# Optimization experiments

Hardware: AMD Instinct MI355X
Metric: run time of the kernel (lower is better)

The kernel has to match this reference:

```python
import jax, jax.numpy as jnp
import numpy as np

EPSILON = 1e-36


def setup_inputs() -> dict:
    key = jax.random.key(0)
    k1, k2, k3, k4 = jax.random.split(key, 4)
    n, in_dim, out_dim = 8192, 128, 128
    x = jax.random.normal(k1, (n, in_dim), dtype=jnp.float32)
    # xavier-uniform-like scale for W_real
    limit = float(np.sqrt(6.0 / (in_dim + out_dim)))
    W_real = jax.random.uniform(k2, (in_dim, out_dim), dtype=jnp.float32, minval=-limit, maxval=limit)
    W_imag = jax.random.uniform(k3, (in_dim, out_dim), dtype=jnp.float32, minval=-0.1, maxval=0.1)
    G = jax.random.uniform(k4, (in_dim, out_dim), dtype=jnp.float32, minval=0.0, maxval=1.0)
    return {"x": x, "W_real": W_real, "W_imag": W_imag, "G": G}


def reference(x, W_real, W_imag, G):
    Gc = jnp.clip(G, 0.0, 1.0)                                   # (i,o)
    # R: (n,i,o) = |x| gated toward 1 by (1-G)
    R = (jnp.abs(x) + EPSILON)[:, :, None] * Gc[None] + (1.0 - Gc)[None]
    # K: pi where x<0, gated by G
    K = jnp.pi * (x < 0).astype(x.dtype)[:, :, None] * Gc[None]  # (n,i,o)
    logR = jnp.log(R)
    A = jnp.einsum('nio,io->no', logR, W_real) - jnp.einsum('nio,io->no', K, W_imag)
    B = jnp.einsum('nio,io->no', logR, W_imag) + jnp.einsum('nio,io->no', K, W_real)
    return jnp.exp(A) * jnp.cos(B)
```

## Files before the change

kernel.cpp:

```cpp
#include <hip/hip_runtime.h>
#include <math.h>


#define NROWS 8192
#define DIM   128
#define RPB   8
#define NT    512
#define RPT   2
#define PI_F  3.14159265358979323846f

typedef float v2f __attribute__((ext_vector_type(2)));

static __device__ __forceinline__ v2f vfma2(v2f a, v2f b, v2f c) {
#if defined(__has_builtin) && __has_builtin(__builtin_elementwise_fma)
    return __builtin_elementwise_fma(a, b, c);
#else
    v2f r; r.x = fmaf(a.x, b.x, c.x); r.y = fmaf(a.y, b.y, c.y); return r;
#endif
}

__global__ __launch_bounds__(256) void prep_w(
    const float* __restrict__ Wr, const float* __restrict__ Wi,
    const float* __restrict__ G, float4* __restrict__ w4)
{
    int t = blockIdx.x * 256 + threadIdx.x;
    if (t < DIM * DIM) {
        float g = fminf(fmaxf(G[t], 0.0f), 1.0f);
        w4[t] = make_float4(g, Wr[t], Wi[t], 0.0f);
    }
}

template <bool PACKED>
__global__ __launch_bounds__(NT, 8) void main_kernel(
    const float* __restrict__ x, const float4* __restrict__ w4,
    const float* __restrict__ Wr, const float* __restrict__ Wi,
    const float* __restrict__ G, float* __restrict__ out)
{
    __shared__ float2 amps[RPB * DIM];
    const int tid   = threadIdx.x;
    const int o     = tid & (DIM - 1);
    const int q     = tid >> 7;
    const int nbase = blockIdx.x * RPB;

    {
        const float2* xr = (const float2*)(x + (size_t)nbase * DIM);
        float2 v = xr[tid];
        float4 s;
        s.x = fabsf(v.x) - 1.0f;  s.y = (v.x < 0.0f) ? PI_F : 0.0f;
        s.z = fabsf(v.y) - 1.0f;  s.w = (v.y < 0.0f) ? PI_F : 0.0f;
        ((float4*)amps)[tid] = s;
    }
    __syncthreads();

    const float2* ap = amps + q * (RPT * DIM);
    v2f aL0 = {0.f,0.f}, aK0 = {0.f,0.f}, aL1 = {0.f,0.f}, aK1 = {0.f,0.f};

#pragma unroll 4
    for (int i = 0; i < DIM; ++i) {
        float g, wr, wi;
        if (PACKED) {
            float4 w = w4[i * DIM + o];
            g = w.x; wr = w.y; wi = w.z;
        } else {
            g  = fminf(fmaxf(G[i * DIM + o], 0.0f), 1.0f);
            wr = Wr[i * DIM + o]; wi = Wi[i * DIM + o];
        }
        const v2f wv = {wr, wi};
        const v2f gv = {g * wi, g * wr};
        float2 a0 = ap[i];
        float2 a1 = ap[DIM + i];
        float t0 = fmaf(a0.x, g, 1.0f);
        float t1 = fmaf(a1.x, g, 1.0f);
        float l0 = __log2f(t0);
        float l1 = __log2f(t1);
        aL0 = vfma2((v2f){l0, l0},     wv, aL0);
        aK0 = vfma2((v2f){a0.y, a0.y}, gv, aK0);
        aL1 = vfma2((v2f){l1, l1},     wv, aL1);
        aK1 = vfma2((v2f){a1.y, a1.y}, gv, aK1);
    }

    const float LN2 = 0.69314718055994530942f;
    {
        float A = fmaf(LN2, aL0.x, -aK0.x);
        float B = fmaf(LN2, aL0.y,  aK0.y);
        out[(size_t)(nbase + q * RPT) * DIM + o] = expf(A) * cosf(B);
    }
    {
        float A = fmaf(LN2, aL1.x, -aK1.x);
        float B = fmaf(LN2, aL1.y,  aK1.y);
        out[(size_t)(nbase + q * RPT + 1) * DIM + o] = expf(A) * cosf(B);
    }
}

extern "C" void kernel_launch(void* const* d_in, const int* in_sizes, int n_in,
                              void* d_out, int out_size, void* d_ws, size_t ws_size,
                              hipStream_t stream) {
    const float* x  = (const float*)d_in[0];
    const float* Wr = (const float*)d_in[1];
    const float* Wi = (const float*)d_in[2];
    const float* G  = (const float*)d_in[3];
    float* out = (float*)d_out;

    const size_t w4_bytes = (size_t)DIM * DIM * sizeof(float4);
    if (ws_size >= w4_bytes) {
        float4* w4 = (float4*)d_ws;
        prep_w<<<(DIM * DIM + 255) / 256, 256, 0, stream>>>(Wr, Wi, G, w4);
        main_kernel<true><<<NROWS / RPB, NT, 0, stream>>>(x, w4, Wr, Wi, G, out);
    } else {
        main_kernel<false><<<NROWS / RPB, NT, 0, stream>>>(x, nullptr, Wr, Wi, G, out);
    }
}
```

Measured before the change: 98.12 us.

## Split reduction dim across thread groups so each weight load serves all eight rows

Each of the four 128-thread groups now handles a quarter of the input dimension for all 8 rows in the block, instead of all 128 inputs for 2 rows. Each weight load is reused across 8 rows rather than 2, and the four partial sums are combined through shared memory before the exp/cos epilogue. Weights are pre-scaled by ln2 and the gated products are precomputed in the prep kernel, and the epilogue uses fast __expf/__cosf intrinsics. In exchange it needs a larger shared buffer, two extra barriers, more accumulator registers and a lower occupancy hint, and the fast intrinsics may lose accuracy for large arguments.

```diff
diff --git a/kernel.cpp b/kernel.cpp
--- a/kernel.cpp
+++ b/kernel.cpp
@@ -6,90 +6,127 @@
 #define DIM   128
 #define RPB   8
 #define NT    512
-#define RPT   2
+#define IQ    32
 #define PI_F  3.14159265358979323846f
+#define LN2_F 0.69314718055994530942f
 
 typedef float v2f __attribute__((ext_vector_type(2)));
 
 static __device__ __forceinline__ v2f vfma2(v2f a, v2f b, v2f c) {
-#if defined(__has_builtin) && __has_builtin(__builtin_elementwise_fma)
     return __builtin_elementwise_fma(a, b, c);
-#else
-    v2f r; r.x = fmaf(a.x, b.x, c.x); r.y = fmaf(a.y, b.y, c.y); return r;
-#endif
 }
 
 __global__ __launch_bounds__(256) void prep_w(
     const float* __restrict__ Wr, const float* __restrict__ Wi,
-    const float* __restrict__ G, float4* __restrict__ w4)
+    const float* __restrict__ G, float4* __restrict__ wq,
+    float* __restrict__ garr)
 {
     int t = blockIdx.x * 256 + threadIdx.x;
     if (t < DIM * DIM) {
-        float g = fminf(fmaxf(G[t], 0.0f), 1.0f);
-        w4[t] = make_float4(g, Wr[t], Wi[t], 0.0f);
+        float g  = fminf(fmaxf(G[t], 0.0f), 1.0f);
+        float wr = Wr[t], wi = Wi[t];
+        wq[t]   = make_float4(LN2_F * wr, LN2_F * wi, -g * wi, g * wr);
+        garr[t] = g;
     }
 }
 
 template <bool PACKED>
-__global__ __launch_bounds__(NT, 8) void main_kernel(
-    const float* __restrict__ x, const float4* __restrict__ w4,
+__global__ __launch_bounds__(NT, 6) void main_kernel(
+    const float* __restrict__ x, const float4* __restrict__ wq,
+    const float* __restrict__ garr,
     const float* __restrict__ Wr, const float* __restrict__ Wi,
     const float* __restrict__ G, float* __restrict__ out)
 {
-    __shared__ float2 amps[RPB * DIM];
+    __shared__ float sbuf[2 * 4 * RPB * DIM];
+    float* am1p = sbuf;
+    float* psp  = sbuf + DIM * RPB;
+
     const int tid   = threadIdx.x;
     const int o     = tid & (DIM - 1);
     const int q     = tid >> 7;
     const int nbase = blockIdx.x * RPB;
+    const float* xb = x + (size_t)nbase * DIM;
 
-    {
-        const float2* xr = (const float2*)(x + (size_t)nbase * DIM);
-        float2 v = xr[tid];
-        float4 s;
-        s.x = fabsf(v.x) - 1.0f;  s.y = (v.x < 0.0f) ? PI_F : 0.0f;
-        s.z = fabsf(v.y) - 1.0f;  s.w = (v.y < 0.0f) ? PI_F : 0.0f;
-        ((float4*)amps)[tid] = s;
+#pragma unroll
+    for (int k = 0; k < 2; ++k) {
+        int e = tid + k * NT;
+        float xv = xb[e];
+        int i = e & (DIM - 1), r = e >> 7;
+        am1p[i * RPB + r] = fabsf(xv) - 1.0f;
+        psp[i * RPB + r]  = (xv < 0.0f) ? PI_F : 0.0f;
     }
     __syncthreads();
 
-    const float2* ap = amps + q * (RPT * DIM);
-    v2f aL0 = {0.f,0.f}, aK0 = {0.f,0.f}, aL1 = {0.f,0.f}, aK1 = {0.f,0.f};
+    v2f accA[4], accB[4];
+#pragma unroll
+    for (int p = 0; p < 4; ++p) { accA[p] = (v2f){0.f, 0.f}; accB[p] = (v2f){0.f, 0.f}; }
 
-#pragma unroll 4
-    for (int i = 0; i < DIM; ++i) {
-        float g, wr, wi;
+    const int ibase = q * IQ;
+#pragma unroll 2
+    for (int ii = 0; ii < IQ; ++ii) {
+        const int i = ibase + ii;
+        float wrl, wil, ngwi, gwr, g;
         if (PACKED) {
-            float4 w = w4[i * DIM + o];
-            g = w.x; wr = w.y; wi = w.z;
+            float4 w = wq[i * DIM + o];
+            g = garr[i * DIM + o];
+            wrl = w.x; wil = w.y; ngwi = w.z; gwr = w.w;
         } else {
-            g  = fminf(fmaxf(G[i * DIM + o], 0.0f), 1.0f);
-            wr = Wr[i * DIM + o]; wi = Wi[i * DIM + o];
+            float wr = Wr[i * DIM + o], wi = Wi[i * DIM + o];
+            g = fminf(fmaxf(G[i * DIM + o], 0.0f), 1.0f);
+            wrl = LN2_F * wr; wil = LN2_F * wi; ngwi = -g * wi; gwr = g * wr;
         }
-        const v2f wv = {wr, wi};
-        const v2f gv = {g * wi, g * wr};
-        float2 a0 = ap[i];
-        float2 a1 = ap[DIM + i];
-        float t0 = fmaf(a0.x, g, 1.0f);
-        float t1 = fmaf(a1.x, g, 1.0f);
-        float l0 = __log2f(t0);
-        float l1 = __log2f(t1);
-        aL0 = vfma2((v2f){l0, l0},     wv, aL0);
-        aK0 = vfma2((v2f){a0.y, a0.y}, gv, aK0);
-        aL1 = vfma2((v2f){l1, l1},     wv, aL1);
-        aK1 = vfma2((v2f){a1.y, a1.y}, gv, aK1);
+        const v2f gg2   = {g, g};
+        const v2f wrl2  = {wrl, wrl};
+        const v2f wil2  = {wil, wil};
+        const v2f ngwi2 = {ngwi, ngwi};
+        const v2f gwr2  = {gwr, gwr};
+        const v2f one2  = {1.0f, 1.0f};
+
+        const float4* a4 = (const float4*)(am1p + i * RPB);
+        const float4* p4 = (const float4*)(psp  + i * RPB);
+        float4 a03 = a4[0], a47 = a4[1];
+        float4 s03 = p4[0], s47 = p4[1];
+
+#define ROWPAIR(mx, my, sx, sy, idx)                                        \
+        do {                                                                \
+            v2f t2 = vfma2((v2f){mx, my}, gg2, one2);                       \
+            v2f l2 = { __log2f(t2.x), __log2f(t2.y) };                      \
+            v2f s2 = {sx, sy};                                              \
+            accA[idx] = vfma2(l2, wrl2, vfma2(s2, ngwi2, accA[idx]));       \
+            accB[idx] = vfma2(l2, wil2, vfma2(s2, gwr2,  accB[idx]));       \
+        } while (0)
+
+        ROWPAIR(a03.x, a03.y, s03.x, s03.y, 0);
+        ROWPAIR(a03.z, a03.w, s03.z, s03.w, 1);
+        ROWPAIR(a47.x, a47.y, s47.x, s47.y, 2);
+        ROWPAIR(a47.z, a47.w, s47.z, s47.w, 3);
+#undef ROWPAIR
     }
 
-    const float LN2 = 0.69314718055994530942f;
-    {
-        float A = fmaf(LN2, aL0.x, -aK0.x);
-        float B = fmaf(LN2, aL0.y,  aK0.y);
-        out[(size_t)(nbase + q * RPT) * DIM + o] = expf(A) * cosf(B);
+    __syncthreads();
+    float* pA = sbuf;
+    float* pB = sbuf + 4 * RPB * DIM;
+#pragma unroll
+    for (int p = 0; p < 4; ++p) {
+        pA[q * (RPB * DIM) + (2 * p) * DIM + o]     = accA[p].x;
+        pA[q * (RPB * DIM) + (2 * p + 1) * DIM + o] = accA[p].y;
+        pB[q * (RPB * DIM) + (2 * p) * DIM + o]     = accB[p].x;
+        pB[q * (RPB * DIM) + (2 * p + 1) * DIM + o] = accB[p].y;
     }
-    {
-        float A = fmaf(LN2, aL1.x, -aK1.x);
-        float B = fmaf(LN2, aL1.y,  aK1.y);
-        out[(size_t)(nbase + q * RPT + 1) * DIM + o] = expf(A) * cosf(B);
+    __syncthreads();
+
+    const int e  = tid * 2;
+    const int r  = e >> 7, oo = e & (DIM - 1);
+    v2f A = {0.f, 0.f}, B = {0.f, 0.f};
+#pragma unroll
+    for (int qq = 0; qq < 4; ++qq) {
+        A += *(const v2f*)&pA[qq * (RPB * DIM) + r * DIM + oo];
+        B += *(const v2f*)&pB[qq * (RPB * DIM) + r * DIM + oo];
     }
+    float2 res;
+    res.x = __expf(A.x) * __cosf(B.x);
+    res.y = __expf(A.y) * __cosf(B.y);
+    *(float2*)&out[(size_t)(nbase + r) * DIM + oo] = res;
 }
 
 extern "C" void kernel_launch(void* const* d_in, const int* in_sizes, int n_in,
@@ -101,12 +138,16 @@
     const float* G  = (const float*)d_in[3];
     float* out = (float*)d_out;
 
-    const size_t w4_bytes = (size_t)DIM * DIM * sizeof(float4);
-    if (ws_size >= w4_bytes) {
-        float4* w4 = (float4*)d_ws;
-        prep_w<<<(DIM * DIM + 255) / 256, 256, 0, stream>>>(Wr, Wi, G, w4);
-        main_kernel<true><<<NROWS / RPB, NT, 0, stream>>>(x, w4, Wr, Wi, G, out);
+    const size_t wq_bytes = (size_t)DIM * DIM * sizeof(float4);
+    const size_t g_bytes  = (size_t)DIM * DIM * sizeof(float);
+    if (ws_size >= wq_bytes + g_bytes) {
+        float4* wq   = (float4*)d_ws;
+        float*  garr = (float*)((char*)d_ws + wq_bytes);
+        prep_w<<<(DIM * DIM + 255) / 256, 256, 0, stream>>>(Wr, Wi, G, wq, garr);
+        main_kernel<true><<<NROWS / RPB, NT, 0, stream>>>(x, wq, garr,
+                                                          nullptr, nullptr, nullptr, out);
     } else {
-        main_kernel<false><<<NROWS / RPB, NT, 0, stream>>>(x, nullptr, Wr, Wi, G, out);
+        main_kernel<false><<<NROWS / RPB, NT, 0, stream>>>(x, nullptr, nullptr,
+                                                           Wr, Wi, G, out);
     }
 }
```

Measured after the change: 86.61 us. 1.13x faster.
